# Optimization experiments

Measured on AMD Instinct MI355X. Metric: run time of the kernel, lower is better.

## Reference

```python
import jax, jax.numpy as jnp
import numpy as np

B, F_NODES, E = 1024, 128, 1024   # graphs, nodes/graph, edges/graph
H, HEADS = 128, 4
HD = H // HEADS


def setup_inputs() -> dict:
    key = jax.random.key(0)
    ks = jax.random.split(key, 24)
    f32 = jnp.float32
    n = jax.random.normal
    d = {
        "x": n(ks[0], (B, F_NODES), f32),
        "edge_index": jax.random.randint(ks[1], (2, E), 0, F_NODES, dtype=jnp.int32),
        # input projection Linear(1, H)
        "w_in": n(ks[2], (1, H), f32) * 0.5,
        "b_in": n(ks[3], (H,), f32) * 0.02,
        # GAT layer 0: heads=4, concat=True, per-head dim HD
        "gat0_w": n(ks[4], (H, H), f32) * (1.0 / np.sqrt(H)),
        "gat0_as": n(ks[5], (HEADS, HD), f32) * 0.1,
        "gat0_ad": n(ks[6], (HEADS, HD), f32) * 0.1,
        "gat0_b": n(ks[7], (H,), f32) * 0.02,
        "bn0_g": 1.0 + 0.1 * n(ks[8], (H,), f32),
        "bn0_b": 0.1 * n(ks[9], (H,), f32),
        "bn0_m": 0.1 * n(ks[10], (H,), f32),
        "bn0_v": 1.0 + 0.1 * jax.random.uniform(ks[11], (H,), f32),
        # GAT layer 1: heads=1, concat=False
        "gat1_w": n(ks[12], (H, H), f32) * (1.0 / np.sqrt(H)),
        "gat1_as": n(ks[13], (1, H), f32) * 0.1,
        "gat1_ad": n(ks[14], (1, H), f32) * 0.1,
        "gat1_b": n(ks[15], (H,), f32) * 0.02,
        "bn1_g": 1.0 + 0.1 * n(ks[16], (H,), f32),
        "bn1_b": 0.1 * n(ks[17], (H,), f32),
        "bn1_m": 0.1 * n(ks[18], (H,), f32),
        "bn1_v": 1.0 + 0.1 * jax.random.uniform(ks[19], (H,), f32),
        # classifier MLP H -> H//2 -> 1
        "w1": n(ks[20], (H, H // 2), f32) * (1.0 / np.sqrt(H)),
        "b1": n(ks[21], (H // 2,), f32) * 0.02,
        "w2": n(ks[22], (H // 2, 1), f32) * (1.0 / np.sqrt(H // 2)),
        "b2": n(ks[23], (1,), f32) * 0.02,
    }
    return d


def _gat(h, src, dst, N, W, a_s, a_d, b, concat):
    # PyG GATConv (shared lin for src/dst, leaky_relu slope 0.2, softmax over dst)
    heads, hd = a_s.shape
    xh = (h @ W).reshape(N, heads, hd)                      # [N, heads, hd]
    e = jax.nn.leaky_relu(
        jnp.sum(xh * a_s[None], -1)[src] + jnp.sum(xh * a_d[None], -1)[dst],
        0.2,
    )                                                        # [Etot, heads]
    m = jax.ops.segment_max(e, dst, num_segments=N)
    ex = jnp.exp(e - m[dst])
    s = jax.ops.segment_sum(ex, dst, num_segments=N)
    alpha = ex / s[dst]
    out = jax.ops.segment_sum(xh[src] * alpha[..., None], dst, num_segments=N)
    out = out.reshape(N, heads * hd) if concat else out[:, 0]
    return out + b


def _bn(h, g, b, m, v):
    return (h - m) / jnp.sqrt(v + 1e-5) * g + b


def reference(x, edge_index, w_in, b_in,
              gat0_w, gat0_as, gat0_ad, gat0_b, bn0_g, bn0_b, bn0_m, bn0_v,
              gat1_w, gat1_as, gat1_ad, gat1_b, bn1_g, bn1_b, bn1_m, bn1_v,
              w1, b1, w2, b2):
    Bsz, Fn = x.shape
    N = Bsz * Fn
    h = jax.nn.relu(x.reshape(N, 1) @ w_in + b_in)           # [N, H]
    # replicate per-graph edges with node offsets, then add self loops
    offs = jnp.arange(Bsz, dtype=edge_index.dtype) * Fn
    eib = (edge_index[:, None, :] + offs[None, :, None]).reshape(2, -1)
    loops = jnp.arange(N, dtype=edge_index.dtype)
    src = jnp.concatenate([eib[0], loops])
    dst = jnp.concatenate([eib[1], loops])
    h = _gat(h, src, dst, N, gat0_w, gat0_as, gat0_ad, gat0_b, True)
    h = jax.nn.relu(_bn(h, bn0_g, bn0_b, bn0_m, bn0_v))
    h = _gat(h, src, dst, N, gat1_w, gat1_as, gat1_ad, gat1_b, False)
    h = jax.nn.relu(_bn(h, bn1_g, bn1_b, bn1_m, bn1_v))
    # global mean pool (each graph has exactly Fn nodes)
    hp = h.reshape(Bsz, Fn, -1).mean(axis=1)                 # [B, H]
    z = jax.nn.relu(hp @ w1 + b1)
    return z @ w2 + b2                                       # [B, 1]
```

## Files before the change

### kernel.cpp

```cpp
#include <hip/hip_runtime.h>

#define FN   128
#define HDIM 128
#define NH   4
#define HSZ  32
#define EB   1024
#define ET   1152
#define RSW  132

typedef __attribute__((ext_vector_type(8))) short bf16x8;
typedef __attribute__((ext_vector_type(4))) float f32x4;
typedef unsigned int u32;
typedef unsigned short u16;

union U8 { bf16x8 v; u32 u[4]; };

__device__ __forceinline__ u32 pack_hl(float v) {
  const u32 u = __float_as_uint(v);
  const u32 hib = u & 0xFFFF0000u;
  const float lo = v - __uint_as_float(hib);
  return hib | (__float_as_uint(lo) >> 16);
}
__device__ __forceinline__ float unpack_val(u32 p) {
  return __uint_as_float(p & 0xFFFF0000u) + __uint_as_float(p << 16);
}
__device__ __forceinline__ float lrelu(float v) {
  return (v > 0.f) ? v : 0.2f * v;
}

__device__ __forceinline__ void unpack_frag(const u32* __restrict__ q,
                                            bf16x8& hi, bf16x8& lo)
{
  const uint4 p0 = *(const uint4*)(q);
  const uint4 p1 = *(const uint4*)(q + 4);
  U8 H, L;
  H.u[0] = (p0.x >> 16) | (p0.y & 0xFFFF0000u);
  L.u[0] = (p0.x & 0xFFFFu) | (p0.y << 16);
  H.u[1] = (p0.z >> 16) | (p0.w & 0xFFFF0000u);
  L.u[1] = (p0.z & 0xFFFFu) | (p0.w << 16);
  H.u[2] = (p1.x >> 16) | (p1.y & 0xFFFF0000u);
  L.u[2] = (p1.x & 0xFFFFu) | (p1.y << 16);
  H.u[3] = (p1.z >> 16) | (p1.w & 0xFFFF0000u);
  L.u[3] = (p1.z & 0xFFFFu) | (p1.w << 16);
  hi = H.v; lo = L.v;
}

__global__ __launch_bounds__(256) void prep_w_kernel(
    const float* __restrict__ g0w, const float* __restrict__ g1w,
    u16* __restrict__ wf)
{
  const int idx = blockIdx.x * 256 + threadIdx.x;
  const int layer = idx >> 14;
  const int r = idx & 16383;
  const int c  = r >> 11;
  const int kc = (r >> 9) & 3;
  const int l  = (r >> 3) & 63;
  const int j  = r & 7;
  const int k = kc * 32 + (l >> 4) * 8 + j;
  const int n = c * 16 + (l & 15);
  const float* W = layer ? g1w : g0w;
  const float v = W[k * HDIM + n];
  const u32 u = __float_as_uint(v);
  const u32 hib = u & 0xFFFF0000u;
  const float lo = v - __uint_as_float(hib);
  wf[layer * 32768 + r]         = (u16)(u >> 16);
  wf[layer * 32768 + 16384 + r] = (u16)(__float_as_uint(lo) >> 16);
}

__device__ __forceinline__ void mfma_gemm_acc(const u32* __restrict__ F,
                                              const u16* __restrict__ wf,
                                              int lw, int lane, f32x4 acc[4][2])
{
  const int cg = lw & 3, rh = lw >> 2;
  const int m = lane & 15, quad = lane >> 4;

  #pragma unroll
  for (int s = 0; s < 4; ++s)
    #pragma unroll
    for (int ct = 0; ct < 2; ++ct) acc[s][ct] = (f32x4){0.f, 0.f, 0.f, 0.f};

  const u16* bbase = wf + (cg * 8) * 512 + lane * 8;

  #pragma unroll
  for (int kc = 0; kc < 4; ++kc) {
    bf16x8 bhi[2], blo[2];
    #pragma unroll
    for (int ct = 0; ct < 2; ++ct) {
      const u16* bp = bbase + ct * 2048 + kc * 512;
      bhi[ct] = *(const bf16x8*)bp;
      blo[ct] = *(const bf16x8*)(bp + 16384);
    }
    #pragma unroll
    for (int s = 0; s < 4; ++s) {
      const u32* ap = F + (rh * 64 + s * 16 + m) * RSW + quad * 8 + kc * 32;
      bf16x8 ahi, alo;
      unpack_frag(ap, ahi, alo);
      #pragma unroll
      for (int ct = 0; ct < 2; ++ct) {
        acc[s][ct] = __builtin_amdgcn_mfma_f32_16x16x32_bf16(ahi, bhi[ct], acc[s][ct], 0, 0, 0);
        acc[s][ct] = __builtin_amdgcn_mfma_f32_16x16x32_bf16(alo, bhi[ct], acc[s][ct], 0, 0, 0);
        acc[s][ct] = __builtin_amdgcn_mfma_f32_16x16x32_bf16(ahi, blo[ct], acc[s][ct], 0, 0, 0);
      }
    }
  }
}

__device__ __forceinline__ void store_acc(float* __restrict__ sg, int lw,
                                          int lane, const f32x4 acc[4][2])
{
  const int cg = lw & 3, rh = lw >> 2;
  const int m = lane & 15, quad = lane >> 4;
  #pragma unroll
  for (int s = 0; s < 4; ++s) {
    const int row0 = rh * 64 + s * 16 + quad * 4;
    #pragma unroll
    for (int ct = 0; ct < 2; ++ct)
      #pragma unroll
      for (int r = 0; r < 4; ++r)
        sg[(row0 + r) * RSW + cg * 32 + ct * 16 + m] = acc[s][ct][r];
  }
}

__global__ __launch_bounds__(1024) void gnn_fused_kernel(
    const float* __restrict__ x, const int* __restrict__ ei,
    const float* __restrict__ w_in, const float* __restrict__ b_in,
    const float* __restrict__ g0as, const float* __restrict__ g0ad,
    const float* __restrict__ g0b,
    const float* __restrict__ bn0g, const float* __restrict__ bn0b,
    const float* __restrict__ bn0m, const float* __restrict__ bn0v,
    const float* __restrict__ g1as, const float* __restrict__ g1ad,
    const float* __restrict__ g1b,
    const float* __restrict__ bn1g, const float* __restrict__ bn1b,
    const float* __restrict__ bn1m, const float* __restrict__ bn1v,
    const float* __restrict__ w1, const float* __restrict__ b1,
    const float* __restrict__ w2, const float* __restrict__ b2,
    const u16* __restrict__ wf,
    float* __restrict__ out)
{
  __shared__ u32   Fb[2 * FN * RSW];
  __shared__ int   s_src[ET];
  __shared__ int   s_rp[FN + 1];
  __shared__ float s_scr[3072];

  const int t = threadIdx.x;
  const int b = blockIdx.x;
  const int g = t >> 9;
  const int u = t & 511;
  const int lane = t & 63;
  const int lw = (t >> 6) & 7;
  u32*   F    = Fb + g * (FN * RSW);
  float* s_es = s_scr + g * 1536;
  float* s_ed = s_es + 512;
  float* s_rs = s_es + 1024;
  f32x4 acc[4][2];

  int* s_deg  = (int*)s_scr;
  int* s_fill = s_deg + 128;
  const int e_dst = ei[EB + t];
  const int e_src = ei[t];
  if (t < 2 * FN) s_deg[t] = 0;
  __syncthreads();
  atomicAdd(&s_deg[e_dst], 1);

  {
    const int j = u & 127, q = u >> 7;
    const float wv = w_in[j], bv = b_in[j];
    const size_t xb = (size_t)(b * 2 + g) * FN;
    for (int n = q * 32; n < q * 32 + 32; ++n) {
      const float v = fmaxf(fmaf(x[xb + n], wv, bv), 0.f);
      F[n * RSW + j] = pack_hl(v);
    }
  }
  __syncthreads();
  if (t < 64) {
    const int v0 = s_deg[2 * t] + 1, v1 = s_deg[2 * t + 1] + 1;
    const int p = v0 + v1;
    int sc = p;
    #pragma unroll
    for (int off = 1; off < 64; off <<= 1) {
      const int o = __shfl_up(sc, off, 64);
      if (t >= off) sc += o;
    }
    s_rp[2 * t] = sc - p;
    s_rp[2 * t + 1] = sc - v1;
    if (t == 63) s_rp[128] = sc;
  }
  __syncthreads();
  {
    const int p = s_rp[e_dst] + atomicAdd(&s_fill[e_dst], 1);
    s_src[p] = e_src | (e_dst << 8);
  }
  if (t < FN) s_src[s_rp[t + 1] - 1] = t | (t << 8);
  __syncthreads();

  mfma_gemm_acc(F, wf, lw, lane, acc);
  __syncthreads();
  store_acc((float*)F, lw, lane, acc);
  __syncthreads();

  {
    const int hh = u >> 7, n = u & 127;
    const float* row = (const float*)F + n * RSW + hh * HSZ;
    float accs = 0.f, accd = 0.f;
    #pragma unroll
    for (int s = 0; s < 8; ++s) {
      const int d = ((n + s) & 7) * 4;
      const float4 v  = *(const float4*)(row + d);
      const float4 as = *(const float4*)(g0as + hh * HSZ + d);
      const float4 ad = *(const float4*)(g0ad + hh * HSZ + d);
      accs += v.x*as.x + v.y*as.y + v.z*as.z + v.w*as.w;
      accd += v.x*ad.x + v.y*ad.y + v.z*ad.z + v.w*ad.w;
    }
    s_es[hh * 128 + n] = accs;
    s_ed[hh * 128 + n] = accd;
  }
  __syncthreads();

  {
    const int hh = u >> 7, n = u & 127;
    const int e0 = s_rp[n], e1 = s_rp[n + 1];
    const float edv = s_ed[hh * 128 + n];
    const float* esb = s_es + hh * 128;
    float sum = 0.f;
    for (int e = e0; e < e1; ++e)
      sum += __expf(lrelu(esb[s_src[e] & 127] + edv));
    s_rs[hh * 128 + n] = 1.f / sum;
  }
  __syncthreads();

  {
    const int cg = u & 15, rg = u >> 4;
    const int c0 = cg * 4, c1 = 64 + cg * 4;
    const int hhA = cg >> 3, hhB = 2 + hhA;
    const float* Ff = (const float*)F;
    const float* esA = s_es + hhA * 128;
    const float* esB = s_es + hhB * 128;
    float4 aA[4], aB[4];
    #pragma unroll
    for (int h2 = 0; h2 < 4; ++h2) {
      const int n = rg + h2 * 32;
      const int e0 = s_rp[n], e1 = s_rp[n + 1];
      const float edvA = s_ed[hhA * 128 + n], edvB = s_ed[hhB * 128 + n];
      const float rsvA = s_rs[hhA * 128 + n], rsvB = s_rs[hhB * 128 + n];
      float4 a0 = make_float4(0.f, 0.f, 0.f, 0.f);
      float4 a1 = make_float4(0.f, 0.f, 0.f, 0.f);
      for (int e = e0; e < e1; ++e) {
        const int s = s_src[e] & 127;
        const float alA = __expf(lrelu(esA[s] + edvA));
        const float alB = __expf(lrelu(esB[s] + edvB));
        const float4 v0 = *(const float4*)(Ff + s * RSW + c0);
        const float4 v1 = *(const float4*)(Ff + s * RSW + c1);
        a0.x = fmaf(alA, v0.x, a0.x); a0.y = fmaf(alA, v0.y, a0.y);
        a0.z = fmaf(alA, v0.z, a0.z); a0.w = fmaf(alA, v0.w, a0.w);
        a1.x = fmaf(alB, v1.x, a1.x); a1.y = fmaf(alB, v1.y, a1.y);
        a1.z = fmaf(alB, v1.z, a1.z); a1.w = fmaf(alB, v1.w, a1.w);
      }
      aA[h2].x = a0.x * rsvA; aA[h2].y = a0.y * rsvA;
      aA[h2].z = a0.z * rsvA; aA[h2].w = a0.w * rsvA;
      aB[h2].x = a1.x * rsvB; aB[h2].y = a1.y * rsvB;
      aB[h2].z = a1.z * rsvB; aB[h2].w = a1.w * rsvB;
    }
    __syncthreads();
    {
      const float4 bb = *(const float4*)&g0b[c0];
      const float4 bm = *(const float4*)&bn0m[c0];
      const float4 bv = *(const float4*)&bn0v[c0];
      const float4 bg = *(const float4*)&bn0g[c0];
      const float4 bt = *(const float4*)&bn0b[c0];
      const float q0 = bg.x * rsqrtf(bv.x + 1e-5f), q1 = bg.y * rsqrtf(bv.y + 1e-5f);
      const float q2 = bg.z * rsqrtf(bv.z + 1e-5f), q3 = bg.w * rsqrtf(bv.w + 1e-5f);
      #pragma unroll
      for (int h2 = 0; h2 < 4; ++h2) {
        const int n = rg + h2 * 32;
        uint4 p;
        p.x = pack_hl(fmaxf((aA[h2].x + bb.x - bm.x) * q0 + bt.x, 0.f));
        p.y = pack_hl(fmaxf((aA[h2].y + bb.y - bm.y) * q1 + bt.y, 0.f));
        p.z = pack_hl(fmaxf((aA[h2].z + bb.z - bm.z) * q2 + bt.z, 0.f));
        p.w = pack_hl(fmaxf((aA[h2].w + bb.w - bm.w) * q3 + bt.w, 0.f));
        *(uint4*)(F + n * RSW + c0) = p;
      }
    }
    {
      const float4 bb = *(const float4*)&g0b[c1];
      const float4 bm = *(const float4*)&bn0m[c1];
      const float4 bv = *(const float4*)&bn0v[c1];
      const float4 bg = *(const float4*)&bn0g[c1];
      const float4 bt = *(const float4*)&bn0b[c1];
      const float q0 = bg.x * rsqrtf(bv.x + 1e-5f), q1 = bg.y * rsqrtf(bv.y + 1e-5f);
      const float q2 = bg.z * rsqrtf(bv.z + 1e-5f), q3 = bg.w * rsqrtf(bv.w + 1e-5f);
      #pragma unroll
      for (int h2 = 0; h2 < 4; ++h2) {
        const int n = rg + h2 * 32;
        uint4 p;
        p.x = pack_hl(fmaxf((aB[h2].x + bb.x - bm.x) * q0 + bt.x, 0.f));
        p.y = pack_hl(fmaxf((aB[h2].y + bb.y - bm.y) * q1 + bt.y, 0.f));
        p.z = pack_hl(fmaxf((aB[h2].z + bb.z - bm.z) * q2 + bt.z, 0.f));
        p.w = pack_hl(fmaxf((aB[h2].w + bb.w - bm.w) * q3 + bt.w, 0.f));
        *(uint4*)(F + n * RSW + c1) = p;
      }
    }
  }
  __syncthreads();

  mfma_gemm_acc(F, wf + 32768, lw, lane, acc);
  __syncthreads();
  store_acc((float*)F, lw, lane, acc);
  __syncthreads();

  {
    const int n = u >> 2, c = u & 3;
    const float* row = (const float*)F + n * RSW + c * 32;
    float accs = 0.f, accd = 0.f;
    #pragma unroll
    for (int i = 0; i < 8; ++i) {
      const int d = i * 4;
      const float4 v  = *(const float4*)(row + d);
      const float4 as = *(const float4*)(g1as + c * 32 + d);
      const float4 ad = *(const float4*)(g1ad + c * 32 + d);
      accs += v.x*as.x + v.y*as.y + v.z*as.z + v.w*as.w;
      accd += v.x*ad.x + v.y*ad.y + v.z*ad.z + v.w*ad.w;
    }
    s_es[u] = accs;
    s_ed[u] = accd;
  }
  __syncthreads();
  if (u < 128) {
    const float* pe = s_es + u * 4;
    const float* pd = s_ed + u * 4;
    s_rs[u]       = pe[0] + pe[1] + pe[2] + pe[3];
    s_rs[128 + u] = pd[0] + pd[1] + pd[2] + pd[3];
  }
  __syncthreads();
  if (u < 128) {
    const int e0 = s_rp[u], e1 = s_rp[u + 1];
    const float edv = s_rs[128 + u];
    float sum = 0.f;
    for (int e = e0; e < e1; ++e)
      sum += __expf(lrelu(s_rs[s_src[e] & 127] + edv));
    s_rs[256 + u] = 1.f / sum;
  }
  __syncthreads();

  {
    const int cg = u & 15, rg = u >> 4;
    const int c0 = cg * 4, c1 = 64 + cg * 4;
    const float* Ff = (const float*)F;
    float4 aA[4], aB[4];
    #pragma unroll
    for (int h2 = 0; h2 < 4; ++h2) {
      const int n = rg + h2 * 32;
      const int e0 = s_rp[n], e1 = s_rp[n + 1];
      const float edv = s_rs[128 + n];
      const float rsv = s_rs[256 + n];
      float4 a0 = make_float4(0.f, 0.f, 0.f, 0.f);
      float4 a1 = make_float4(0.f, 0.f, 0.f, 0.f);
      for (int e = e0; e < e1; ++e) {
        const int s = s_src[e] & 127;
        const float al = __expf(lrelu(s_rs[s] + edv));
        const float4 v0 = *(const float4*)(Ff + s * RSW + c0);
        const float4 v1 = *(const float4*)(Ff + s * RSW + c1);
        a0.x = fmaf(al, v0.x, a0.x); a0.y = fmaf(al, v0.y, a0.y);
        a0.z = fmaf(al, v0.z, a0.z); a0.w = fmaf(al, v0.w, a0.w);
        a1.x = fmaf(al, v1.x, a1.x); a1.y = fmaf(al, v1.y, a1.y);
        a1.z = fmaf(al, v1.z, a1.z); a1.w = fmaf(al, v1.w, a1.w);
      }
      aA[h2].x = a0.x * rsv; aA[h2].y = a0.y * rsv;
      aA[h2].z = a0.z * rsv; aA[h2].w = a0.w * rsv;
      aB[h2].x = a1.x * rsv; aB[h2].y = a1.y * rsv;
      aB[h2].z = a1.z * rsv; aB[h2].w = a1.w * rsv;
    }
    __syncthreads();
    {
      const float4 bb = *(const float4*)&g1b[c0];
      const float4 bm = *(const float4*)&bn1m[c0];
      const float4 bv = *(const float4*)&bn1v[c0];
      const float4 bg = *(const float4*)&bn1g[c0];
      const float4 bt = *(const float4*)&bn1b[c0];
      const float q0 = bg.x * rsqrtf(bv.x + 1e-5f), q1 = bg.y * rsqrtf(bv.y + 1e-5f);
      const float q2 = bg.z * rsqrtf(bv.z + 1e-5f), q3 = bg.w * rsqrtf(bv.w + 1e-5f);
      #pragma unroll
      for (int h2 = 0; h2 < 4; ++h2) {
        const int n = rg + h2 * 32;
        uint4 p;
        p.x = pack_hl(fmaxf((aA[h2].x + bb.x - bm.x) * q0 + bt.x, 0.f));
        p.y = pack_hl(fmaxf((aA[h2].y + bb.y - bm.y) * q1 + bt.y, 0.f));
        p.z = pack_hl(fmaxf((aA[h2].z + bb.z - bm.z) * q2 + bt.z, 0.f));
        p.w = pack_hl(fmaxf((aA[h2].w + bb.w - bm.w) * q3 + bt.w, 0.f));
        *(uint4*)(F + n * RSW + c0) = p;
      }
    }
    {
      const float4 bb = *(const float4*)&g1b[c1];
      const float4 bm = *(const float4*)&bn1m[c1];
      const float4 bv = *(const float4*)&bn1v[c1];
      const float4 bg = *(const float4*)&bn1g[c1];
      const float4 bt = *(const float4*)&bn1b[c1];
      const float q0 = bg.x * rsqrtf(bv.x + 1e-5f), q1 = bg.y * rsqrtf(bv.y + 1e-5f);
      const float q2 = bg.z * rsqrtf(bv.z + 1e-5f), q3 = bg.w * rsqrtf(bv.w + 1e-5f);
      #pragma unroll
      for (int h2 = 0; h2 < 4; ++h2) {
        const int n = rg + h2 * 32;
        uint4 p;
        p.x = pack_hl(fmaxf((aB[h2].x + bb.x - bm.x) * q0 + bt.x, 0.f));
        p.y = pack_hl(fmaxf((aB[h2].y + bb.y - bm.y) * q1 + bt.y, 0.f));
        p.z = pack_hl(fmaxf((aB[h2].z + bb.z - bm.z) * q2 + bt.z, 0.f));
        p.w = pack_hl(fmaxf((aB[h2].w + bb.w - bm.w) * q3 + bt.w, 0.f));
        *(uint4*)(F + n * RSW + c1) = p;
      }
    }
  }
  __syncthreads();

  {
    const int j = u & 127, q = u >> 7;
    float p = 0.f;
    for (int n = q * 32; n < q * 32 + 32; ++n) p += unpack_val(F[n * RSW + j]);
    s_es[q * 128 + j] = p;
  }
  __syncthreads();
  if (u < 128) {
    s_ed[u] = (s_es[u] + s_es[u + 128] + s_es[u + 256] + s_es[u + 384])
              * (1.f / 128.f);
  }
  __syncthreads();
  {
    const int j = u & 63, part = u >> 6;
    float a = 0.f;
    #pragma unroll
    for (int k = part * 16; k < part * 16 + 16; ++k)
      a = fmaf(s_ed[k], w1[k * 64 + j], a);
    s_rs[part * 64 + j] = a;
  }
  __syncthreads();
  if (u < 64) {
    float a = b1[u];
    #pragma unroll
    for (int p = 0; p < 8; ++p) a += s_rs[p * 64 + u];
    a = fmaxf(a, 0.f);
    float v = a * w2[u];
    #pragma unroll
    for (int off = 32; off > 0; off >>= 1) v += __shfl_down(v, off, 64);
    if (u == 0) out[b * 2 + g] = v + b2[0];
  }
}

extern "C" void kernel_launch(void* const* d_in, const int* in_sizes, int n_in,
                              void* d_out, int out_size, void* d_ws, size_t ws_size,
                              hipStream_t stream)
{
  const float* x    = (const float*)d_in[0];
  const int*   ei   = (const int*)d_in[1];
  const float* w_in = (const float*)d_in[2];
  const float* b_in = (const float*)d_in[3];
  const float* g0w  = (const float*)d_in[4];
  const float* g0as = (const float*)d_in[5];
  const float* g0ad = (const float*)d_in[6];
  const float* g0b  = (const float*)d_in[7];
  const float* bn0g = (const float*)d_in[8];
  const float* bn0b = (const float*)d_in[9];
  const float* bn0m = (const float*)d_in[10];
  const float* bn0v = (const float*)d_in[11];
  const float* g1w  = (const float*)d_in[12];
  const float* g1as = (const float*)d_in[13];
  const float* g1ad = (const float*)d_in[14];
  const float* g1b  = (const float*)d_in[15];
  const float* bn1g = (const float*)d_in[16];
  const float* bn1b = (const float*)d_in[17];
  const float* bn1m = (const float*)d_in[18];
  const float* bn1v = (const float*)d_in[19];
  const float* w1   = (const float*)d_in[20];
  const float* b1   = (const float*)d_in[21];
  const float* w2   = (const float*)d_in[22];
  const float* b2   = (const float*)d_in[23];

  u16* wf = (u16*)d_ws;

  prep_w_kernel<<<128, 256, 0, stream>>>(g0w, g1w, wf);
  gnn_fused_kernel<<<512, 1024, 0, stream>>>(x, ei, w_in, b_in,
      g0as, g0ad, g0b, bn0g, bn0b, bn0m, bn0v,
      g1as, g1ad, g1b, bn1g, bn1b, bn1m, bn1v,
      w1, b1, w2, b2, wf, (float*)d_out);
}
```

Before: 195.4 us.

## Fuse softmax denominator into aggregation and precompute folded BN constants

Each thread now owns one (node, 32-column head slice): it computes the softmax denominator and then aggregates the 32 columns in the same pass. This removes a separate barrier-separated phase and recomputes each edge's attention weight once per head instead of once per four-column group. Bias and batch-norm parameters are folded once into per-column scale and shift values held in shared memory. In exchange each thread keeps 32 accumulators, which raises register pressure. Same-row LDS reads across lanes may also change bank-conflict behaviour.

```diff
diff --git a/kernel.cpp b/kernel.cpp
--- a/kernel.cpp
+++ b/kernel.cpp
@@ -141,6 +141,7 @@
   __shared__ int   s_src[ET];
   __shared__ int   s_rp[FN + 1];
   __shared__ float s_scr[3072];
+  __shared__ float s_bn[512];
 
   const int t = threadIdx.x;
   const int b = blockIdx.x;
@@ -184,6 +185,17 @@
     s_rp[2 * t] = sc - p;
     s_rp[2 * t + 1] = sc - v1;
     if (t == 63) s_rp[128] = sc;
+  } else if (t >= 512 && t < 768) {
+    const int layer = (t >> 7) & 1;
+    const int col = t & 127;
+    const float bb = layer ? g1b[col]  : g0b[col];
+    const float bm = layer ? bn1m[col] : bn0m[col];
+    const float bv = layer ? bn1v[col] : bn0v[col];
+    const float bg = layer ? bn1g[col] : bn0g[col];
+    const float bt = layer ? bn1b[col] : bn0b[col];
+    const float q = bg * rsqrtf(bv + 1e-5f);
+    s_bn[layer * 256 + col] = q;
+    s_bn[layer * 256 + 128 + col] = (bb - bm) * q + bt;
   }
   __syncthreads();
   {
@@ -217,87 +229,42 @@
   __syncthreads();
 
   {
-    const int hh = u >> 7, n = u & 127;
+    const int n = u & 127, hh = u >> 7;
+    const int cb = hh * HSZ;
+    const float* Ff = (const float*)F;
     const int e0 = s_rp[n], e1 = s_rp[n + 1];
     const float edv = s_ed[hh * 128 + n];
     const float* esb = s_es + hh * 128;
     float sum = 0.f;
     for (int e = e0; e < e1; ++e)
       sum += __expf(lrelu(esb[s_src[e] & 127] + edv));
-    s_rs[hh * 128 + n] = 1.f / sum;
-  }
-  __syncthreads();
-
-  {
-    const int cg = u & 15, rg = u >> 4;
-    const int c0 = cg * 4, c1 = 64 + cg * 4;
-    const int hhA = cg >> 3, hhB = 2 + hhA;
-    const float* Ff = (const float*)F;
-    const float* esA = s_es + hhA * 128;
-    const float* esB = s_es + hhB * 128;
-    float4 aA[4], aB[4];
-    #pragma unroll
-    for (int h2 = 0; h2 < 4; ++h2) {
-      const int n = rg + h2 * 32;
-      const int e0 = s_rp[n], e1 = s_rp[n + 1];
-      const float edvA = s_ed[hhA * 128 + n], edvB = s_ed[hhB * 128 + n];
-      const float rsvA = s_rs[hhA * 128 + n], rsvB = s_rs[hhB * 128 + n];
-      float4 a0 = make_float4(0.f, 0.f, 0.f, 0.f);
-      float4 a1 = make_float4(0.f, 0.f, 0.f, 0.f);
-      for (int e = e0; e < e1; ++e) {
-        const int s = s_src[e] & 127;
-        const float alA = __expf(lrelu(esA[s] + edvA));
-        const float alB = __expf(lrelu(esB[s] + edvB));
-        const float4 v0 = *(const float4*)(Ff + s * RSW + c0);
-        const float4 v1 = *(const float4*)(Ff + s * RSW + c1);
-        a0.x = fmaf(alA, v0.x, a0.x); a0.y = fmaf(alA, v0.y, a0.y);
-        a0.z = fmaf(alA, v0.z, a0.z); a0.w = fmaf(alA, v0.w, a0.w);
-        a1.x = fmaf(alB, v1.x, a1.x); a1.y = fmaf(alB, v1.y, a1.y);
-        a1.z = fmaf(alB, v1.z, a1.z); a1.w = fmaf(alB, v1.w, a1.w);
+    const float rsv = 1.f / sum;
+    float4 a[8];
+    #pragma unroll
+    for (int i = 0; i < 8; ++i) a[i] = make_float4(0.f, 0.f, 0.f, 0.f);
+    for (int e = e0; e < e1; ++e) {
+      const int s = s_src[e] & 127;
+      const float al = __expf(lrelu(esb[s] + edv));
+      const float* rp_ = Ff + s * RSW + cb;
+      #pragma unroll
+      for (int i = 0; i < 8; ++i) {
+        const float4 vv = *(const float4*)(rp_ + i * 4);
+        a[i].x = fmaf(al, vv.x, a[i].x); a[i].y = fmaf(al, vv.y, a[i].y);
+        a[i].z = fmaf(al, vv.z, a[i].z); a[i].w = fmaf(al, vv.w, a[i].w);
       }
-      aA[h2].x = a0.x * rsvA; aA[h2].y = a0.y * rsvA;
-      aA[h2].z = a0.z * rsvA; aA[h2].w = a0.w * rsvA;
-      aB[h2].x = a1.x * rsvB; aB[h2].y = a1.y * rsvB;
-      aB[h2].z = a1.z * rsvB; aB[h2].w = a1.w * rsvB;
     }
     __syncthreads();
-    {
-      const float4 bb = *(const float4*)&g0b[c0];
-      const float4 bm = *(const float4*)&bn0m[c0];
-      const float4 bv = *(const float4*)&bn0v[c0];
-      const float4 bg = *(const float4*)&bn0g[c0];
-      const float4 bt = *(const float4*)&bn0b[c0];
-      const float q0 = bg.x * rsqrtf(bv.x + 1e-5f), q1 = bg.y * rsqrtf(bv.y + 1e-5f);
-      const float q2 = bg.z * rsqrtf(bv.z + 1e-5f), q3 = bg.w * rsqrtf(bv.w + 1e-5f);
-      #pragma unroll
-      for (int h2 = 0; h2 < 4; ++h2) {
-        const int n = rg + h2 * 32;
-        uint4 p;
-        p.x = pack_hl(fmaxf((aA[h2].x + bb.x - bm.x) * q0 + bt.x, 0.f));
-        p.y = pack_hl(fmaxf((aA[h2].y + bb.y - bm.y) * q1 + bt.y, 0.f));
-        p.z = pack_hl(fmaxf((aA[h2].z + bb.z - bm.z) * q2 + bt.z, 0.f));
-        p.w = pack_hl(fmaxf((aA[h2].w + bb.w - bm.w) * q3 + bt.w, 0.f));
-        *(uint4*)(F + n * RSW + c0) = p;
-      }
-    }
-    {
-      const float4 bb = *(const float4*)&g0b[c1];
-      const float4 bm = *(const float4*)&bn0m[c1];
-      const float4 bv = *(const float4*)&bn0v[c1];
-      const float4 bg = *(const float4*)&bn0g[c1];
-      const float4 bt = *(const float4*)&bn0b[c1];
-      const float q0 = bg.x * rsqrtf(bv.x + 1e-5f), q1 = bg.y * rsqrtf(bv.y + 1e-5f);
-      const float q2 = bg.z * rsqrtf(bv.z + 1e-5f), q3 = bg.w * rsqrtf(bv.w + 1e-5f);
-      #pragma unroll
-      for (int h2 = 0; h2 < 4; ++h2) {
-        const int n = rg + h2 * 32;
-        uint4 p;
-        p.x = pack_hl(fmaxf((aB[h2].x + bb.x - bm.x) * q0 + bt.x, 0.f));
-        p.y = pack_hl(fmaxf((aB[h2].y + bb.y - bm.y) * q1 + bt.y, 0.f));
-        p.z = pack_hl(fmaxf((aB[h2].z + bb.z - bm.z) * q2 + bt.z, 0.f));
-        p.w = pack_hl(fmaxf((aB[h2].w + bb.w - bm.w) * q3 + bt.w, 0.f));
-        *(uint4*)(F + n * RSW + c1) = p;
-      }
+    #pragma unroll
+    for (int i = 0; i < 8; ++i) {
+      const int col = cb + i * 4;
+      const float4 q = *(const float4*)&s_bn[col];
+      const float4 r = *(const float4*)&s_bn[128 + col];
+      uint4 p;
+      p.x = pack_hl(fmaxf(fmaf(a[i].x * rsv, q.x, r.x), 0.f));
+      p.y = pack_hl(fmaxf(fmaf(a[i].y * rsv, q.y, r.y), 0.f));
+      p.z = pack_hl(fmaxf(fmaf(a[i].z * rsv, q.z, r.z), 0.f));
+      p.w = pack_hl(fmaxf(fmaf(a[i].w * rsv, q.w, r.w), 0.f));
+      *(uint4*)(F + n * RSW + col) = p;
     }
   }
   __syncthreads();
@@ -331,82 +298,43 @@
     s_rs[128 + u] = pd[0] + pd[1] + pd[2] + pd[3];
   }
   __syncthreads();
-  if (u < 128) {
-    const int e0 = s_rp[u], e1 = s_rp[u + 1];
-    const float edv = s_rs[128 + u];
+
+  {
+    const int n = u & 127, cg = u >> 7;
+    const int cb = cg * HSZ;
+    const float* Ff = (const float*)F;
+    const int e0 = s_rp[n], e1 = s_rp[n + 1];
+    const float edv = s_rs[128 + n];
     float sum = 0.f;
     for (int e = e0; e < e1; ++e)
       sum += __expf(lrelu(s_rs[s_src[e] & 127] + edv));
-    s_rs[256 + u] = 1.f / sum;
-  }
-  __syncthreads();
-
-  {
-    const int cg = u & 15, rg = u >> 4;
-    const int c0 = cg * 4, c1 = 64 + cg * 4;
-    const float* Ff = (const float*)F;
-    float4 aA[4], aB[4];
-    #pragma unroll
-    for (int h2 = 0; h2 < 4; ++h2) {
-      const int n = rg + h2 * 32;
-      const int e0 = s_rp[n], e1 = s_rp[n + 1];
-      const float edv = s_rs[128 + n];
-      const float rsv = s_rs[256 + n];
-      float4 a0 = make_float4(0.f, 0.f, 0.f, 0.f);
-      float4 a1 = make_float4(0.f, 0.f, 0.f, 0.f);
-      for (int e = e0; e < e1; ++e) {
-        const int s = s_src[e] & 127;
-        const float al = __expf(lrelu(s_rs[s] + edv));
-        const float4 v0 = *(const float4*)(Ff + s * RSW + c0);
-        const float4 v1 = *(const float4*)(Ff + s * RSW + c1);
-        a0.x = fmaf(al, v0.x, a0.x); a0.y = fmaf(al, v0.y, a0.y);
-        a0.z = fmaf(al, v0.z, a0.z); a0.w = fmaf(al, v0.w, a0.w);
-        a1.x = fmaf(al, v1.x, a1.x); a1.y = fmaf(al, v1.y, a1.y);
-        a1.z = fmaf(al, v1.z, a1.z); a1.w = fmaf(al, v1.w, a1.w);
+    const float rsv = 1.f / sum;
+    float4 a[8];
+    #pragma unroll
+    for (int i = 0; i < 8; ++i) a[i] = make_float4(0.f, 0.f, 0.f, 0.f);
+    for (int e = e0; e < e1; ++e) {
+      const int s = s_src[e] & 127;
+      const float al = __expf(lrelu(s_rs[s] + edv));
+      const float* rp_ = Ff + s * RSW + cb;
+      #pragma unroll
+      for (int i = 0; i < 8; ++i) {
+        const float4 vv = *(const float4*)(rp_ + i * 4);
+        a[i].x = fmaf(al, vv.x, a[i].x); a[i].y = fmaf(al, vv.y, a[i].y);
+        a[i].z = fmaf(al, vv.z, a[i].z); a[i].w = fmaf(al, vv.w, a[i].w);
       }
-      aA[h2].x = a0.x * rsv; aA[h2].y = a0.y * rsv;
-      aA[h2].z = a0.z * rsv; aA[h2].w = a0.w * rsv;
-      aB[h2].x = a1.x * rsv; aB[h2].y = a1.y * rsv;
-      aB[h2].z = a1.z * rsv; aB[h2].w = a1.w * rsv;
     }
     __syncthreads();
-    {
-      const float4 bb = *(const float4*)&g1b[c0];
-      const float4 bm = *(const float4*)&bn1m[c0];
-      const float4 bv = *(const float4*)&bn1v[c0];
-      const float4 bg = *(const float4*)&bn1g[c0];
-      const float4 bt = *(const float4*)&bn1b[c0];
-      const float q0 = bg.x * rsqrtf(bv.x + 1e-5f), q1 = bg.y * rsqrtf(bv.y + 1e-5f);
-      const float q2 = bg.z * rsqrtf(bv.z + 1e-5f), q3 = bg.w * rsqrtf(bv.w + 1e-5f);
-      #pragma unroll
-      for (int h2 = 0; h2 < 4; ++h2) {
-        const int n = rg + h2 * 32;
-        uint4 p;
-        p.x = pack_hl(fmaxf((aA[h2].x + bb.x - bm.x) * q0 + bt.x, 0.f));
-        p.y = pack_hl(fmaxf((aA[h2].y + bb.y - bm.y) * q1 + bt.y, 0.f));
-        p.z = pack_hl(fmaxf((aA[h2].z + bb.z - bm.z) * q2 + bt.z, 0.f));
-        p.w = pack_hl(fmaxf((aA[h2].w + bb.w - bm.w) * q3 + bt.w, 0.f));
-        *(uint4*)(F + n * RSW + c0) = p;
-      }
-    }
-    {
-      const float4 bb = *(const float4*)&g1b[c1];
-      const float4 bm = *(const float4*)&bn1m[c1];
-      const float4 bv = *(const float4*)&bn1v[c1];
-      const float4 bg = *(const float4*)&bn1g[c1];
-      const float4 bt = *(const float4*)&bn1b[c1];
-      const float q0 = bg.x * rsqrtf(bv.x + 1e-5f), q1 = bg.y * rsqrtf(bv.y + 1e-5f);
-      const float q2 = bg.z * rsqrtf(bv.z + 1e-5f), q3 = bg.w * rsqrtf(bv.w + 1e-5f);
-      #pragma unroll
-      for (int h2 = 0; h2 < 4; ++h2) {
-        const int n = rg + h2 * 32;
-        uint4 p;
-        p.x = pack_hl(fmaxf((aB[h2].x + bb.x - bm.x) * q0 + bt.x, 0.f));
-        p.y = pack_hl(fmaxf((aB[h2].y + bb.y - bm.y) * q1 + bt.y, 0.f));
-        p.z = pack_hl(fmaxf((aB[h2].z + bb.z - bm.z) * q2 + bt.z, 0.f));
-        p.w = pack_hl(fmaxf((aB[h2].w + bb.w - bm.w) * q3 + bt.w, 0.f));
-        *(uint4*)(F + n * RSW + c1) = p;
-      }
+    #pragma unroll
+    for (int i = 0; i < 8; ++i) {
+      const int col = cb + i * 4;
+      const float4 q = *(const float4*)&s_bn[256 + col];
+      const float4 r = *(const float4*)&s_bn[384 + col];
+      uint4 p;
+      p.x = pack_hl(fmaxf(fmaf(a[i].x * rsv, q.x, r.x), 0.f));
+      p.y = pack_hl(fmaxf(fmaf(a[i].y * rsv, q.y, r.y), 0.f));
+      p.z = pack_hl(fmaxf(fmaf(a[i].z * rsv, q.z, r.z), 0.f));
+      p.w = pack_hl(fmaxf(fmaf(a[i].w * rsv, q.w, r.w), 0.f));
+      *(uint4*)(F + n * RSW + col) = p;
     }
   }
   __syncthreads();
```

Result: no change. 192.6 us (-1.5%).
